# Kernel optimization log

Hardware: AMD Instinct MI355X
Metric: run time of the kernel (lower is better)

## Reference

```python
import jax, jax.numpy as jnp
import numpy as np

N_S = 50000
N_T = 50000
D_IN = 256
D_OUT = 128
E = 1600000


def setup_inputs() -> dict:
    key = jax.random.key(0)
    ks = jax.random.split(key, 7)
    inp_s = jax.random.normal(ks[0], (N_S, D_IN), dtype=jnp.float32)
    inp_t = jax.random.normal(ks[1], (N_T, D_IN), dtype=jnp.float32)
    adj_s_idx = jax.random.randint(ks[2], (E, 2), 0, N_S, dtype=jnp.int32)
    adj_s_val = jax.random.uniform(ks[3], (E,), dtype=jnp.float32)
    adj_t_idx = jax.random.randint(ks[4], (E, 2), 0, N_T, dtype=jnp.int32)
    adj_t_val = jax.random.uniform(ks[5], (E,), dtype=jnp.float32)
    # Glorot-uniform shared weights, as in weight_variable_glorot
    init_range = np.sqrt(6.0 / (D_IN + D_OUT))
    W = jax.random.uniform(ks[6], (D_IN, D_OUT), minval=-init_range,
                           maxval=init_range, dtype=jnp.float32)
    return {"inp_s": inp_s, "inp_t": inp_t,
            "adj_s_idx": adj_s_idx, "adj_s_val": adj_s_val,
            "adj_t_idx": adj_t_idx, "adj_t_val": adj_t_val,
            "W": W}


def _spmm(idx, val, x, n_rows):
    # sparse [n_rows, n_cols] @ dense x: gather source rows, scale, scatter-add to dest
    rows, cols = idx[:, 0], idx[:, 1]
    msgs = x[cols] * val[:, None]                      # [E, D_OUT]
    return jax.ops.segment_sum(msgs, rows, num_segments=n_rows)


def _gcn_branch(x, idx, val, W, n_rows):
    # dropout = 0.0 -> identity; dense GEMM -> SpMM -> relu
    h = x @ W                                          # [N, D_OUT]
    h = _spmm(idx, val, h, n_rows)
    return jax.nn.relu(h)


def reference(inp_s, inp_t, adj_s_idx, adj_s_val, adj_t_idx, adj_t_val, W):
    out_s = _gcn_branch(inp_s, adj_s_idx, adj_s_val, W, N_S)
    out_t = _gcn_branch(inp_t, adj_t_idx, adj_t_val, W, N_T)
    return (out_s, out_t)
```

## Files before the change

kernel.cpp:

```cpp
#include <hip/hip_runtime.h>
#include <cstdint>
#include <cstddef>

#define D_IN   256
#define D_OUT  128
#define NB_MAX 256
#define KV_CAP 12288
#define NCB    8

typedef short bf16x8 __attribute__((ext_vector_type(8)));
typedef float f32x4  __attribute__((ext_vector_type(4)));

union Frag { bf16x8 v; uint32_t u[4]; };

struct Branch {
  const float* X;
  const int*   idx;
  const float* val;
  uint16_t* H;
  int*   ptr;
  int*   bucketCur;
  uint64_t* kv2;
  uint32_t* csr4;
  float* out;
};

__device__ inline uint32_t cvt_pk_bf16(float lo, float hi) {
  uint32_t r;
  asm("v_cvt_pk_bf16_f32 %0, %1, %2" : "=v"(r) : "v"(lo), "v"(hi));
  return r;
}

__device__ inline int block_scan256_excl(int v, int tid) {
  int lane = tid & 63, w = tid >> 6;
  int s = v;
  #pragma unroll
  for (int off = 1; off < 64; off <<= 1) {
    int t = __shfl_up(s, off);
    if (lane >= off) s += t;
  }
  __shared__ int wsum[4];
  if (lane == 63) wsum[w] = s;
  __syncthreads();
  int add = 0;
  #pragma unroll
  for (int i = 0; i < 4; ++i) add += (i < w) ? wsum[i] : 0;
  return s + add - v;
}

__global__ __launch_bounds__(256) void wprep3_kernel(const float* __restrict__ W,
                                                     uint16_t* __restrict__ WT3) {
  int n = blockIdx.x;
  int t = threadIdx.x;
  int ks = t >> 5, g = (t >> 3) & 3, j = t & 7;
  int k = ks * 32 + ((j < 4) ? (4 * g + j) : (16 + 4 * g + (j - 4)));
  uint32_t u = __float_as_uint(W[k * 128 + n]);
  WT3[(size_t)((ks * 4 + g) * 128 + n) * 8 + j] =
      (uint16_t)((u + 0x7FFFu + ((u >> 16) & 1u)) >> 16);
}

__global__ __launch_bounds__(256) void bin_kernel(Branch b0, Branch b1, int ne, int nb) {
  Branch b = blockIdx.y ? b1 : b0;
  __shared__ int hist[NB_MAX];
  __shared__ int lcur[NB_MAX];
  __shared__ int gbase[NB_MAX];
  const int t = threadIdx.x;
  const int base = blockIdx.x * 4096;
  if (base >= ne) return;
  if (t < nb) hist[t] = 0;
  __syncthreads();
  uint64_t kv2[16];
  int bkt[16];
  #pragma unroll
  for (int i = 0; i < 16; ++i) {
    int e = base + i * 256 + t;
    bkt[i] = -1;
    if (e < ne) {
      int2 rc = ((const int2*)b.idx)[e];
      uint32_t v = __float_as_uint(b.val[e]);
      kv2[i] = ((uint64_t)v << 32) | ((uint32_t)rc.x << 16) | (uint32_t)rc.y;
      bkt[i] = rc.x >> 8;
      atomicAdd(&hist[bkt[i]], 1);
    }
  }
  __syncthreads();
  if (t < nb) {
    int h = hist[t];
    gbase[t] = h ? atomicAdd(&b.bucketCur[t], h) : 0;
    lcur[t] = 0;
  }
  __syncthreads();
  #pragma unroll
  for (int i = 0; i < 16; ++i) {
    if (bkt[i] >= 0) {
      int pos = gbase[bkt[i]] + atomicAdd(&lcur[bkt[i]], 1);
      if (pos < KV_CAP)
        b.kv2[(size_t)bkt[i] * KV_CAP + pos] = kv2[i];
    }
  }
}

__global__ __launch_bounds__(256) void gemm_kernel(const uint16_t* __restrict__ WT3,
                                                   Branch b0, Branch b1, int n_rows) {
  Branch b = blockIdx.y ? b1 : b0;
  const int t = threadIdx.x;
  const int w = t >> 6, l = t & 63;
  const int c = l & 15, g = l >> 4;
  const int row0 = blockIdx.x * 128;
  if (row0 >= n_rows) return;

  __shared__ uint8_t sX[4][16384];

  auto stage = [&](int ks, int buf) {
    #pragma unroll
    for (int i = 0; i < 4; ++i) {
      int row = i * 32 + (t >> 3);
      int gr = row0 + row; if (gr > n_rows - 1) gr = n_rows - 1;
      int kb = ((t & 7) * 16) ^ ((row & 7) << 4);
      const float* src = b.X + (size_t)gr * D_IN + ks * 32 + (kb >> 2);
      __builtin_amdgcn_global_load_lds(
          (const __attribute__((address_space(1))) uint32_t*)src,
          (__attribute__((address_space(3))) uint32_t*)&sX[buf][i * 4096 + t * 16],
          16, 0, 0);
    }
  };

  const uint4* Bp = (const uint4*)WT3;
  uint4 bu[2][8];
  auto loadB = [&](int ks, int set) {
    #pragma unroll
    for (int nf = 0; nf < 8; ++nf)
      bu[set][nf] = Bp[(ks * 4 + g) * 128 + nf * 16 + c];
  };

  f32x4 acc[2][8];
  #pragma unroll
  for (int i = 0; i < 2; ++i)
    #pragma unroll
    for (int j = 0; j < 8; ++j) acc[i][j] = (f32x4){0.f, 0.f, 0.f, 0.f};

  stage(0, 0);
  loadB(0, 0);
  stage(1, 1);
  loadB(1, 1);
  stage(2, 2);

  #pragma unroll
  for (int ks = 0; ks < 8; ++ks) {
    if (ks < 6)       asm volatile("s_waitcnt vmcnt(16)" ::: "memory");
    else if (ks == 6) asm volatile("s_waitcnt vmcnt(12)" ::: "memory");
    else              asm volatile("s_waitcnt vmcnt(0)"  ::: "memory");
    __builtin_amdgcn_s_barrier();

    Frag A[2];
    #pragma unroll
    for (int rf = 0; rf < 2; ++rf) {
      int row = w * 32 + rf * 16 + c;
      const uint8_t* base = &sX[ks & 3][row * 128];
      int swz = (row & 7) << 4;
      float4 x0 = *(const float4*)(base + ((g * 16) ^ swz));
      float4 x1 = *(const float4*)(base + ((64 + g * 16) ^ swz));
      A[rf].u[0] = cvt_pk_bf16(x0.x, x0.y);
      A[rf].u[1] = cvt_pk_bf16(x0.z, x0.w);
      A[rf].u[2] = cvt_pk_bf16(x1.x, x1.y);
      A[rf].u[3] = cvt_pk_bf16(x1.z, x1.w);
    }

    #pragma unroll
    for (int nf = 0; nf < 8; ++nf) {
      Frag B;
      B.u[0] = bu[ks & 1][nf].x; B.u[1] = bu[ks & 1][nf].y;
      B.u[2] = bu[ks & 1][nf].z; B.u[3] = bu[ks & 1][nf].w;
      acc[0][nf] = __builtin_amdgcn_mfma_f32_16x16x32_bf16(A[0].v, B.v, acc[0][nf], 0, 0, 0);
      acc[1][nf] = __builtin_amdgcn_mfma_f32_16x16x32_bf16(A[1].v, B.v, acc[1][nf], 0, 0, 0);
    }

    if (ks < 6) loadB(ks + 2, ks & 1);
    if (ks < 5) stage(ks + 3, (ks + 3) & 3);
  }

  #pragma unroll
  for (int rf = 0; rf < 2; ++rf)
    #pragma unroll
    for (int nf = 0; nf < 8; ++nf)
      #pragma unroll
      for (int r = 0; r < 4; ++r) {
        float v = acc[rf][nf][r];
        float o = __shfl_xor(v, 1);
        uint32_t pk = cvt_pk_bf16(v, o);
        uint32_t pk2 = __shfl_xor(pk, 2);
        int row_g = row0 + w * 32 + rf * 16 + 4 * g + r;
        if ((c & 3) == 0 && row_g < n_rows) {
          uint2 d; d.x = pk; d.y = pk2;
          *(uint2*)(b.H + (size_t)row_g * D_OUT + nf * 16 + c) = d;
        }
      }
}

__global__ __launch_bounds__(256) void bucket_csr_kernel(Branch b0, Branch b1, int n, int nb) {
  Branch b = blockIdx.y ? b1 : b0;
  const int bkt = blockIdx.x;
  const int tid = threadIdx.x;
  __shared__ int sbase[NB_MAX];
  __shared__ int hist2[256 * NCB];
  __shared__ int cur2[256 * NCB];

  int cntv = (tid < nb) ? b.bucketCur[tid] : 0;
  if (cntv > KV_CAP) cntv = KV_CAP;
  int excl0 = block_scan256_excl(cntv, tid);
  if (tid < nb) sbase[tid] = excl0;
  if (bkt == 0 && tid == nb - 1) b.ptr[n] = excl0 + cntv;
  __syncthreads();

  const int dstBase = sbase[bkt];
  int cnt = b.bucketCur[bkt];
  if (cnt > KV_CAP) cnt = KV_CAP;
  const uint64_t* src = b.kv2 + (size_t)bkt * KV_CAP;

  #pragma unroll
  for (int i = 0; i < NCB; ++i) hist2[i * 256 + tid] = 0;
  __syncthreads();
  for (int e = tid; e < cnt; e += 256) {
    uint64_t kv = src[e];
    int lr = (int)((kv >> 16) & 0xFF);
    int cb = (int)(kv & 0xFFFFu) >> 13;
    atomicAdd(&hist2[lr * NCB + cb], 1);
  }
  __syncthreads();

  int h[NCB], rowtot = 0;
  #pragma unroll
  for (int j = 0; j < NCB; ++j) { h[j] = hist2[tid * NCB + j]; rowtot += h[j]; }
  int rowExcl = block_scan256_excl(rowtot, tid);
  int row = bkt * 256 + tid;
  if (row < n) b.ptr[row] = dstBase + rowExcl;
  int run = dstBase + rowExcl;
  #pragma unroll
  for (int j = 0; j < NCB; ++j) { cur2[tid * NCB + j] = run; run += h[j]; }
  __syncthreads();

  for (int e = tid; e < cnt; e += 256) {
    uint64_t kv = src[e];
    int lr = (int)((kv >> 16) & 0xFF);
    uint32_t col = (uint32_t)(kv & 0xFFFFu);
    int cb = (int)col >> 13;
    uint32_t u = (uint32_t)(kv >> 32);
    uint32_t vbf = (u + 0x7FFFu + ((u >> 16) & 1u)) & 0xFFFF0000u;
    int pos = atomicAdd(&cur2[lr * NCB + cb], 1);
    b.csr4[pos] = vbf | col;
  }
}

__global__ __launch_bounds__(256) void gather_kernel(Branch b0, Branch b1, int n_rows) {
  const int bid = blockIdx.x;
  const int br  = (bid & 7) >> 2;
  const int local = (bid >> 3) * 4 + (bid & 3);
  Branch b = br ? b1 : b0;
  int row = local * 16 + (threadIdx.x >> 4);
  if (row >= n_rows) return;
  int lane4 = threadIdx.x & 15;
  const uint4* Hq = (const uint4*)b.H;
  int beg = b.ptr[row], end = b.ptr[row + 1];
  float4 acc0 = make_float4(0.f, 0.f, 0.f, 0.f);
  float4 acc1 = make_float4(0.f, 0.f, 0.f, 0.f);

  auto fma_h = [&](uint32_t k, uint4 h) {
    float v = __uint_as_float(k & 0xFFFF0000u);
    float f0 = __uint_as_float(h.x << 16), f1 = __uint_as_float(h.x & 0xFFFF0000u);
    float f2 = __uint_as_float(h.y << 16), f3 = __uint_as_float(h.y & 0xFFFF0000u);
    float f4 = __uint_as_float(h.z << 16), f5 = __uint_as_float(h.z & 0xFFFF0000u);
    float f6 = __uint_as_float(h.w << 16), f7 = __uint_as_float(h.w & 0xFFFF0000u);
    acc0.x = fmaf(f0, v, acc0.x); acc0.y = fmaf(f1, v, acc0.y);
    acc0.z = fmaf(f2, v, acc0.z); acc0.w = fmaf(f3, v, acc0.w);
    acc1.x = fmaf(f4, v, acc1.x); acc1.y = fmaf(f5, v, acc1.y);
    acc1.z = fmaf(f6, v, acc1.z); acc1.w = fmaf(f7, v, acc1.w);
  };

  int e = beg;
  for (; e + 8 <= end; e += 8) {
    uint32_t k[8];
    #pragma unroll
    for (int i = 0; i < 8; ++i) k[i] = b.csr4[e + i];
    uint4 h[8];
    #pragma unroll
    for (int i = 0; i < 8; ++i)
      h[i] = Hq[(size_t)(k[i] & 0xFFFFu) * 16 + lane4];
    #pragma unroll
    for (int i = 0; i < 8; ++i) fma_h(k[i], h[i]);
  }
  for (; e < end; ++e) {
    uint32_t k = b.csr4[e];
    uint4 h = Hq[(size_t)(k & 0xFFFFu) * 16 + lane4];
    fma_h(k, h);
  }

  float4 o0, o1;
  o0.x = fmaxf(acc0.x, 0.f); o0.y = fmaxf(acc0.y, 0.f);
  o0.z = fmaxf(acc0.z, 0.f); o0.w = fmaxf(acc0.w, 0.f);
  o1.x = fmaxf(acc1.x, 0.f); o1.y = fmaxf(acc1.y, 0.f);
  o1.z = fmaxf(acc1.z, 0.f); o1.w = fmaxf(acc1.w, 0.f);
  float* orow = b.out + (size_t)row * D_OUT + lane4 * 8;
  *(float4*)orow = o0;
  *(float4*)(orow + 4) = o1;
}

extern "C" void kernel_launch(void* const* d_in, const int* in_sizes, int n_in,
                              void* d_out, int out_size, void* d_ws, size_t ws_size,
                              hipStream_t stream) {
  const float* inp_s = (const float*)d_in[0];
  const float* inp_t = (const float*)d_in[1];
  const int*   idx_s = (const int*)d_in[2];
  const float* val_s = (const float*)d_in[3];
  const int*   idx_t = (const int*)d_in[4];
  const float* val_t = (const float*)d_in[5];
  const float* W     = (const float*)d_in[6];
  float* out = (float*)d_out;

  const int n  = in_sizes[0] / D_IN;
  const int ne = in_sizes[3];
  const int nb = (n + 255) >> 8;

  char* p = (char*)d_ws;
  auto alloc = [&](size_t bytes) -> char* {
    char* r = p;
    p += (bytes + 255) & ~(size_t)255;
    return r;
  };
  uint16_t* H_s    = (uint16_t*)alloc((size_t)n * D_OUT * 2);
  uint16_t* H_t    = (uint16_t*)alloc((size_t)n * D_OUT * 2);
  uint16_t* WT3    = (uint16_t*)alloc((size_t)128 * 256 * 2);
  int* ptr_s       = (int*)alloc((size_t)(n + 1) * 4);
  int* ptr_t       = (int*)alloc((size_t)(n + 1) * 4);
  int* bcur        = (int*)alloc((size_t)2 * NB_MAX * 4);
  int* bcur_s      = bcur;
  int* bcur_t      = bcur + NB_MAX;
  uint64_t* kv2_s  = (uint64_t*)alloc((size_t)NB_MAX * KV_CAP * 8);
  uint64_t* kv2_t  = (uint64_t*)alloc((size_t)NB_MAX * KV_CAP * 8);
  uint32_t* c4_s   = (uint32_t*)alloc((size_t)ne * 4);
  uint32_t* c4_t   = (uint32_t*)alloc((size_t)ne * 4);

  Branch bs = { inp_s, idx_s, val_s, H_s, ptr_s, bcur_s, kv2_s, c4_s, out };
  Branch bt = { inp_t, idx_t, val_t, H_t, ptr_t, bcur_t, kv2_t, c4_t,
                out + (size_t)n * D_OUT };

  const int nblkE = (ne + 4095) / 4096;
  const int nblkG = (n + 127) / 128;
  const int bpb   = (((n + 15) / 16) + 3) & ~3;

  hipMemsetAsync(bcur, 0, (size_t)2 * NB_MAX * 4, stream);
  wprep3_kernel<<<dim3(128), 256, 0, stream>>>(W, WT3);
  bin_kernel<<<dim3(nblkE, 2), 256, 0, stream>>>(bs, bt, ne, nb);
  gemm_kernel<<<dim3(nblkG, 2), 256, 0, stream>>>(WT3, bs, bt, n);
  bucket_csr_kernel<<<dim3(nb, 2), 256, 0, stream>>>(bs, bt, n, nb);
  gather_kernel<<<dim3(2 * bpb), 256, 0, stream>>>(bs, bt, n);
}
```

Baseline: 200.6 us.

## Split gather into column-band passes with cooperative grid sync for cache locality

Edges within each CSR row are now grouped into 4 column bands instead of 8 sub-buckets, and per-row band offsets are written to a new ptr2 array. A cooperative persistent gather kernel (512 blocks, 13 row chunks per thread group, accumulators kept in registers) processes one band per pass, with a grid-wide sync between passes, so all blocks read the same slice of H at the same time. This aims to keep the gathered H rows resident in L2/LLC rather than streaming randomly across the whole table. The costs are grid syncs, heavy register pressure from 26 float4 accumulators, and fewer blocks in flight. If the cooperative launch fails it falls back to the old gather kernel.

```diff
diff --git a/kernel.cpp b/kernel.cpp
--- a/kernel.cpp
+++ b/kernel.cpp
@@ -1,12 +1,17 @@
 #include <hip/hip_runtime.h>
+#include <hip/hip_cooperative_groups.h>
 #include <cstdint>
 #include <cstddef>
+
+namespace cg = cooperative_groups;
 
 #define D_IN   256
 #define D_OUT  128
 #define NB_MAX 256
 #define KV_CAP 12288
-#define NCB    8
+#define NPASS  4
+#define GBLK   512
+#define NCHUNK 13
 
 typedef short bf16x8 __attribute__((ext_vector_type(8)));
 typedef float f32x4  __attribute__((ext_vector_type(4)));
@@ -19,6 +24,7 @@
   const float* val;
   uint16_t* H;
   int*   ptr;
+  int*   ptr2;
   int*   bucketCur;
   uint64_t* kv2;
   uint32_t* csr4;
@@ -197,13 +203,14 @@
       }
 }
 
-__global__ __launch_bounds__(256) void bucket_csr_kernel(Branch b0, Branch b1, int n, int nb) {
+__global__ __launch_bounds__(256) void bucket_csr_kernel(Branch b0, Branch b1, int n, int nb,
+                                                         float binv) {
   Branch b = blockIdx.y ? b1 : b0;
   const int bkt = blockIdx.x;
   const int tid = threadIdx.x;
   __shared__ int sbase[NB_MAX];
-  __shared__ int hist2[256 * NCB];
-  __shared__ int cur2[256 * NCB];
+  __shared__ int hist2[256 * NPASS];
+  __shared__ int cur2[256 * NPASS];
 
   int cntv = (tid < nb) ? b.bucketCur[tid] : 0;
   if (cntv > KV_CAP) cntv = KV_CAP;
@@ -217,37 +224,114 @@
   if (cnt > KV_CAP) cnt = KV_CAP;
   const uint64_t* src = b.kv2 + (size_t)bkt * KV_CAP;
 
-  #pragma unroll
-  for (int i = 0; i < NCB; ++i) hist2[i * 256 + tid] = 0;
+  auto bandof = [&](uint32_t col) {
+    int cb = (int)((float)col * binv);
+    return cb > NPASS - 1 ? NPASS - 1 : cb;
+  };
+
+  #pragma unroll
+  for (int i = 0; i < NPASS; ++i) hist2[i * 256 + tid] = 0;
   __syncthreads();
   for (int e = tid; e < cnt; e += 256) {
     uint64_t kv = src[e];
     int lr = (int)((kv >> 16) & 0xFF);
-    int cb = (int)(kv & 0xFFFFu) >> 13;
-    atomicAdd(&hist2[lr * NCB + cb], 1);
-  }
-  __syncthreads();
-
-  int h[NCB], rowtot = 0;
-  #pragma unroll
-  for (int j = 0; j < NCB; ++j) { h[j] = hist2[tid * NCB + j]; rowtot += h[j]; }
+    atomicAdd(&hist2[lr * NPASS + bandof((uint32_t)(kv & 0xFFFFu))], 1);
+  }
+  __syncthreads();
+
+  int h[NPASS], rowtot = 0;
+  #pragma unroll
+  for (int j = 0; j < NPASS; ++j) { h[j] = hist2[tid * NPASS + j]; rowtot += h[j]; }
   int rowExcl = block_scan256_excl(rowtot, tid);
   int row = bkt * 256 + tid;
   if (row < n) b.ptr[row] = dstBase + rowExcl;
   int run = dstBase + rowExcl;
   #pragma unroll
-  for (int j = 0; j < NCB; ++j) { cur2[tid * NCB + j] = run; run += h[j]; }
+  for (int j = 0; j < NPASS; ++j) {
+    cur2[tid * NPASS + j] = run;
+    if (row < n) b.ptr2[row * NPASS + j] = run;
+    run += h[j];
+  }
   __syncthreads();
 
   for (int e = tid; e < cnt; e += 256) {
     uint64_t kv = src[e];
     int lr = (int)((kv >> 16) & 0xFF);
     uint32_t col = (uint32_t)(kv & 0xFFFFu);
-    int cb = (int)col >> 13;
     uint32_t u = (uint32_t)(kv >> 32);
     uint32_t vbf = (u + 0x7FFFu + ((u >> 16) & 1u)) & 0xFFFF0000u;
-    int pos = atomicAdd(&cur2[lr * NCB + cb], 1);
+    int pos = atomicAdd(&cur2[lr * NPASS + bandof(col)], 1);
     b.csr4[pos] = vbf | col;
+  }
+}
+
+__global__ __launch_bounds__(256, 2) void gather_coop_kernel(Branch b0, Branch b1, int n_rows) {
+  cg::grid_group grid = cg::this_grid();
+  const int bid = blockIdx.x;
+  const int br  = (bid & 7) >> 2;
+  const int local = (bid >> 3) * 4 + (bid & 3);
+  Branch b = br ? b1 : b0;
+  const int lane4 = threadIdx.x & 15;
+  const int rgrp  = threadIdx.x >> 4;
+  const uint4* Hq = (const uint4*)b.H;
+
+  float4 a0[NCHUNK], a1[NCHUNK];
+  #pragma unroll
+  for (int ch = 0; ch < NCHUNK; ++ch) {
+    a0[ch] = make_float4(0.f, 0.f, 0.f, 0.f);
+    a1[ch] = make_float4(0.f, 0.f, 0.f, 0.f);
+  }
+
+  for (int pass = 0; pass < NPASS; ++pass) {
+    #pragma unroll
+    for (int ch = 0; ch < NCHUNK; ++ch) {
+      int row = (local * NCHUNK + ch) * 16 + rgrp;
+      if (row < n_rows) {
+        int e0 = b.ptr2[row * NPASS + pass];
+        int e1 = (pass == NPASS - 1) ? b.ptr[row + 1] : b.ptr2[row * NPASS + pass + 1];
+        auto fma_h = [&](uint32_t k, uint4 h) {
+          float v = __uint_as_float(k & 0xFFFF0000u);
+          float f0 = __uint_as_float(h.x << 16), f1 = __uint_as_float(h.x & 0xFFFF0000u);
+          float f2 = __uint_as_float(h.y << 16), f3 = __uint_as_float(h.y & 0xFFFF0000u);
+          float f4 = __uint_as_float(h.z << 16), f5 = __uint_as_float(h.z & 0xFFFF0000u);
+          float f6 = __uint_as_float(h.w << 16), f7 = __uint_as_float(h.w & 0xFFFF0000u);
+          a0[ch].x = fmaf(f0, v, a0[ch].x); a0[ch].y = fmaf(f1, v, a0[ch].y);
+          a0[ch].z = fmaf(f2, v, a0[ch].z); a0[ch].w = fmaf(f3, v, a0[ch].w);
+          a1[ch].x = fmaf(f4, v, a1[ch].x); a1[ch].y = fmaf(f5, v, a1[ch].y);
+          a1[ch].z = fmaf(f6, v, a1[ch].z); a1[ch].w = fmaf(f7, v, a1[ch].w);
+        };
+        int e = e0;
+        for (; e + 4 <= e1; e += 4) {
+          uint32_t k0 = b.csr4[e + 0], k1 = b.csr4[e + 1];
+          uint32_t k2 = b.csr4[e + 2], k3 = b.csr4[e + 3];
+          uint4 h0 = Hq[(size_t)(k0 & 0xFFFFu) * 16 + lane4];
+          uint4 h1 = Hq[(size_t)(k1 & 0xFFFFu) * 16 + lane4];
+          uint4 h2 = Hq[(size_t)(k2 & 0xFFFFu) * 16 + lane4];
+          uint4 h3 = Hq[(size_t)(k3 & 0xFFFFu) * 16 + lane4];
+          fma_h(k0, h0); fma_h(k1, h1); fma_h(k2, h2); fma_h(k3, h3);
+        }
+        for (; e < e1; ++e) {
+          uint32_t k = b.csr4[e];
+          fma_h(k, Hq[(size_t)(k & 0xFFFFu) * 16 + lane4]);
+        }
+      }
+    }
+    if (pass < NPASS - 1) grid.sync();
+  }
+
+  #pragma unroll
+  for (int ch = 0; ch < NCHUNK; ++ch) {
+    int row = (local * NCHUNK + ch) * 16 + rgrp;
+    if (row < n_rows) {
+      float4 o0, o1;
+      o0.x = fmaxf(a0[ch].x, 0.f); o0.y = fmaxf(a0[ch].y, 0.f);
+      o0.z = fmaxf(a0[ch].z, 0.f); o0.w = fmaxf(a0[ch].w, 0.f);
+      o1.x = fmaxf(a1[ch].x, 0.f); o1.y = fmaxf(a1[ch].y, 0.f);
+      o1.z = fmaxf(a1[ch].z, 0.f); o1.w = fmaxf(a1[ch].w, 0.f);
+      float* orow = b.out + (size_t)row * D_OUT + lane4 * 8;
+      *(float4*)orow = o0;
+      *(float4*)(orow + 4) = o1;
+    }
   }
 }
 
@@ -331,6 +415,8 @@
   uint16_t* WT3    = (uint16_t*)alloc((size_t)128 * 256 * 2);
   int* ptr_s       = (int*)alloc((size_t)(n + 1) * 4);
   int* ptr_t       = (int*)alloc((size_t)(n + 1) * 4);
+  int* ptr2_s      = (int*)alloc((size_t)n * NPASS * 4);
+  int* ptr2_t      = (int*)alloc((size_t)n * NPASS * 4);
   int* bcur        = (int*)alloc((size_t)2 * NB_MAX * 4);
   int* bcur_s      = bcur;
   int* bcur_t      = bcur + NB_MAX;
@@ -339,18 +425,26 @@
   uint32_t* c4_s   = (uint32_t*)alloc((size_t)ne * 4);
   uint32_t* c4_t   = (uint32_t*)alloc((size_t)ne * 4);
 
-  Branch bs = { inp_s, idx_s, val_s, H_s, ptr_s, bcur_s, kv2_s, c4_s, out };
-  Branch bt = { inp_t, idx_t, val_t, H_t, ptr_t, bcur_t, kv2_t, c4_t,
+  Branch bs = { inp_s, idx_s, val_s, H_s, ptr_s, ptr2_s, bcur_s, kv2_s, c4_s, out };
+  Branch bt = { inp_t, idx_t, val_t, H_t, ptr_t, ptr2_t, bcur_t, kv2_t, c4_t,
                 out + (size_t)n * D_OUT };
 
   const int nblkE = (ne + 4095) / 4096;
   const int nblkG = (n + 127) / 128;
   const int bpb   = (((n + 15) / 16) + 3) & ~3;
+  const float binv = (float)NPASS / (float)n;
 
   hipMemsetAsync(bcur, 0, (size_t)2 * NB_MAX * 4, stream);
   wprep3_kernel<<<dim3(128), 256, 0, stream>>>(W, WT3);
   bin_kernel<<<dim3(nblkE, 2), 256, 0, stream>>>(bs, bt, ne, nb);
   gemm_kernel<<<dim3(nblkG, 2), 256, 0, stream>>>(WT3, bs, bt, n);
-  bucket_csr_kernel<<<dim3(nb, 2), 256, 0, stream>>>(bs, bt, n, nb);
-  gather_kernel<<<dim3(2 * bpb), 256, 0, stream>>>(bs, bt, n);
-}
+  bucket_csr_kernel<<<dim3(nb, 2), 256, 0, stream>>>(bs, bt, n, nb, binv);
+
+  int n_arg = n;
+  void* args[] = { (void*)&bs, (void*)&bt, (void*)&n_arg };
+  hipError_t cerr = hipLaunchCooperativeKernel((void*)gather_coop_kernel, dim3(GBLK),
+                                               dim3(256), args, 0, stream);
+  if (cerr != hipSuccess) {
+    gather_kernel<<<dim3(2 * bpb), 256, 0, stream>>>(bs, bt, n);
+  }
+}
```

Result: slower. 489.3 us (+143.9%).
